# Kernel tuning notes

Measured on AMD Instinct MI355X. Metric: run time of the kernel, lower is better.

The kernel has to match this reference:

```python
import jax, jax.numpy as jnp
import numpy as np

UNITS = 1024
D = 1024

def setup_inputs() -> dict:
    key = jax.random.key(0)
    ks = jax.random.split(key, 8)
    B, T = 32, 2048
    query = jax.random.normal(ks[0], (B, D), dtype=jnp.float32)
    values = jax.random.normal(ks[1], (B, T, D), dtype=jnp.float32)
    s1 = 1.0 / np.sqrt(D)
    s2 = 1.0 / np.sqrt(UNITS)
    W1 = jax.random.normal(ks[2], (D, UNITS), dtype=jnp.float32) * s1
    b1 = jnp.zeros((UNITS,), dtype=jnp.float32)
    W2 = jax.random.normal(ks[3], (D, UNITS), dtype=jnp.float32) * s1
    b2 = jnp.zeros((UNITS,), dtype=jnp.float32)
    Wv = jax.random.normal(ks[4], (UNITS, 1), dtype=jnp.float32) * s2
    bv = jnp.zeros((1,), dtype=jnp.float32)
    return {"query": query, "values": values, "W1": W1, "b1": b1,
            "W2": W2, "b2": b2, "Wv": Wv, "bv": bv}

def reference(query, values, W1, b1, W2, b2, Wv, bv):
    # query: [B, D]; values: [B, T, D]
    q_proj = query @ W1 + b1                     # [B, U]
    v_proj = jnp.einsum('btd,du->btu', values, W2) + b2  # [B, T, U]
    h = jnp.tanh(q_proj[:, None, :] + v_proj)    # [B, T, U]
    score = jnp.einsum('btu,uo->bto', h, Wv) + bv  # [B, T, 1]
    attention_weights = jax.nn.softmax(score, axis=1)  # [B, T, 1]
    context_vector = jnp.sum(attention_weights * values, axis=1)  # [B, D]
    return (context_vector, attention_weights)
```

## Files before the change

### kernel.cpp

```cpp
#include <hip/hip_runtime.h>
#include <hip/hip_bf16.h>
#include <stdint.h>


typedef unsigned short ushort_t;
typedef short bf16x8 __attribute__((ext_vector_type(8)));
typedef float f32x4 __attribute__((ext_vector_type(4)));

#define GLOBAL_AS __attribute__((address_space(1)))
#define LDS_AS    __attribute__((address_space(3)))

__device__ __forceinline__ ushort_t f2bf(float f) {
    union { float f; unsigned int u; } v;
    v.f = f;
    unsigned int u = v.u;
    unsigned int r = u + 0x7FFFu + ((u >> 16) & 1u);
    return (ushort_t)(r >> 16);
}
__device__ __forceinline__ unsigned int pk2(float a, float b) {
    union { __hip_bfloat162 h; unsigned int u; } c;
    c.h = __float22bfloat162_rn(make_float2(a, b));
    return c.u;
}
__device__ __forceinline__ float fast_tanh(float x) {
    float ax = __builtin_fabsf(x);
    float e = __expf(-2.0f * ax);
    float t = (1.0f - e) * __builtin_amdgcn_rcpf(1.0f + e);
    return __builtin_copysignf(t, x);
}

static constexpr int B_ = 32, T_ = 2048, D_ = 1024, U_ = 1024;
static constexpr int M_ = B_ * T_;

__global__ __launch_bounds__(256) void k_convert(const float* __restrict__ v,
                                                 ushort_t* __restrict__ o) {
    size_t i = ((size_t)blockIdx.x * 256 + threadIdx.x) * 8;
    f32x4 a = *(const f32x4*)(v + i);
    f32x4 b = *(const f32x4*)(v + i + 4);
    uint4 p;
    p.x = pk2(a[0], a[1]);
    p.y = pk2(a[2], a[3]);
    p.z = pk2(b[0], b[1]);
    p.w = pk2(b[2], b[3]);
    *(uint4*)(o + i) = p;
}

__global__ __launch_bounds__(256) void k_transpose_w2(const float* __restrict__ W2,
                                                      ushort_t* __restrict__ W2T) {
    __shared__ float tile[32][33];
    int u0 = blockIdx.x * 32, d0 = blockIdx.y * 32;
    int tx = threadIdx.x & 31, ty = threadIdx.x >> 5;
#pragma unroll
    for (int r = 0; r < 4; ++r) {
        int dd = ty + r * 8;
        tile[dd][tx] = W2[(size_t)(d0 + dd) * U_ + (u0 + tx)];
    }
    __syncthreads();
#pragma unroll
    for (int r = 0; r < 4; ++r) {
        int uu = ty + r * 8;
        W2T[(size_t)(u0 + uu) * D_ + (d0 + tx)] = f2bf(tile[tx][uu]);
    }
}

__global__ __launch_bounds__(256) void k_qproj(const float* __restrict__ query,
                                               const float* __restrict__ W1,
                                               const float* __restrict__ b1,
                                               const float* __restrict__ b2,
                                               float* __restrict__ qpb) {
    int b = blockIdx.y;
    int u = blockIdx.x * 256 + threadIdx.x;
    __shared__ float qs[D_];
    for (int i = threadIdx.x; i < D_; i += 256) qs[i] = query[b * D_ + i];
    __syncthreads();
    float acc = 0.f;
#pragma unroll 8
    for (int d = 0; d < D_; ++d) acc += qs[d] * W1[(size_t)d * U_ + u];
    qpb[b * U_ + u] = acc + b1[u] + b2[u];
}

#define BM 128
#define BN 128
#define BK 64

__global__ __launch_bounds__(256) void k_score_gemm(const ushort_t* __restrict__ Vbf,
                                                    const ushort_t* __restrict__ W2T,
                                                    const float* __restrict__ qpb,
                                                    const float* __restrict__ Wv,
                                                    float* __restrict__ scores_partial) {
    __shared__ ushort_t As[BM * BK];
    __shared__ ushort_t Bs[BN * BK];
    __shared__ float sScore[BM];

    const int tid = threadIdx.x;
    const int lane = tid & 63;
    const int w = tid >> 6;
    const int wm = w >> 1;
    const int wn = w & 1;

    const int g = blockIdx.x;
    const int mt = ((g >> 6) << 3) | (g & 7);
    const int nt = (g >> 3) & 7;
    const int m0 = mt * BM;
    const int n0 = nt * BN;

    if (tid < BM) sScore[tid] = 0.f;

    f32x4 acc[4][4];
#pragma unroll
    for (int i = 0; i < 4; ++i)
#pragma unroll
        for (int j = 0; j < 4; ++j) acc[i][j] = (f32x4){0.f, 0.f, 0.f, 0.f};

    const int lr = lane >> 3;
    const int c = (lane & 7) ^ lr;
    const ushort_t* aBase = Vbf + (size_t)(m0 + w * 8 + lr) * D_ + c * 8;
    const ushort_t* bBase = W2T + (size_t)(n0 + w * 8 + lr) * D_ + c * 8;

    const int quad = lane >> 4;
    const int l15 = lane & 15;
    const int l7 = l15 & 7;

    for (int k0 = 0; k0 < D_; k0 += BK) {
#pragma unroll
        for (int i = 0; i < 4; ++i) {
            __builtin_amdgcn_global_load_lds(
                (const GLOBAL_AS void*)(aBase + k0 + (size_t)i * 32 * D_),
                (LDS_AS void*)(As + i * 2048 + w * 512), 16, 0, 0);
        }
#pragma unroll
        for (int i = 0; i < 4; ++i) {
            __builtin_amdgcn_global_load_lds(
                (const GLOBAL_AS void*)(bBase + k0 + (size_t)i * 32 * D_),
                (LDS_AS void*)(Bs + i * 2048 + w * 512), 16, 0, 0);
        }
        __syncthreads();
#pragma unroll
        for (int kk = 0; kk < BK; kk += 32) {
            bf16x8 af[4], bfr[4];
            const int cb = kk >> 3;
#pragma unroll
            for (int i = 0; i < 4; ++i) {
                int r = wm * 64 + i * 16 + l15;
                af[i] = *(const bf16x8*)(As + (r << 6) + ((((quad + cb) ^ l7)) << 3));
            }
#pragma unroll
            for (int j = 0; j < 4; ++j) {
                int r = wn * 64 + j * 16 + l15;
                bfr[j] = *(const bf16x8*)(Bs + (r << 6) + ((((quad + cb) ^ l7)) << 3));
            }
#pragma unroll
            for (int i = 0; i < 4; ++i)
#pragma unroll
                for (int j = 0; j < 4; ++j)
                    acc[i][j] = __builtin_amdgcn_mfma_f32_16x16x32_bf16(
                        af[i], bfr[j], acc[i][j], 0, 0, 0);
        }
        __syncthreads();
    }

    const int b = m0 >> 11;
    const float* qp = qpb + b * U_;
    float qv[4], wv[4];
#pragma unroll
    for (int j = 0; j < 4; ++j) {
        int u = n0 + wn * 64 + j * 16 + l15;
        qv[j] = qp[u];
        wv[j] = Wv[u];
    }
#pragma unroll
    for (int i = 0; i < 4; ++i) {
#pragma unroll
        for (int r = 0; r < 4; ++r) {
            float s = 0.f;
#pragma unroll
            for (int j = 0; j < 4; ++j) s += fast_tanh(acc[i][j][r] + qv[j]) * wv[j];
            s += __shfl_xor(s, 1);
            s += __shfl_xor(s, 2);
            s += __shfl_xor(s, 4);
            s += __shfl_xor(s, 8);
            if (l15 == 0) atomicAdd(&sScore[wm * 64 + i * 16 + quad * 4 + r], s);
        }
    }
    __syncthreads();
    if (tid < BM) scores_partial[(size_t)(m0 + tid) * 8 + nt] = sScore[tid];
}

__global__ __launch_bounds__(256) void k_score_gemm_f32(const float* __restrict__ values,
                                                        const ushort_t* __restrict__ W2T,
                                                        const float* __restrict__ qpb,
                                                        const float* __restrict__ Wv,
                                                        float* __restrict__ scores_partial) {
    __shared__ ushort_t As[BM * BK];
    __shared__ ushort_t Bs[BN * BK];
    __shared__ float sScore[BM];

    const int tid = threadIdx.x;
    const int lane = tid & 63;
    const int w = tid >> 6;
    const int wm = w >> 1;
    const int wn = w & 1;
    const int n0 = blockIdx.x * BN;
    const int m0 = blockIdx.y * BM;

    if (tid < BM) sScore[tid] = 0.f;

    f32x4 acc[4][4];
#pragma unroll
    for (int i = 0; i < 4; ++i)
#pragma unroll
        for (int j = 0; j < 4; ++j) acc[i][j] = (f32x4){0.f, 0.f, 0.f, 0.f};

    const int rr = tid >> 4;
    const int cc = tid & 15;
    const float* aSrc = values + (size_t)(m0 + rr) * D_ + cc * 4;
    ushort_t* aDst = As + rr * BK + cc * 4;

    const int mB = lane >> 3;
    const int kB = (lane & 7) * 8;
    const ushort_t* bBase = W2T + (size_t)(n0 + w * 8 + mB) * D_ + kB;

    const int quad = lane >> 4;
    const int l15 = lane & 15;

    for (int k0 = 0; k0 < D_; k0 += BK) {
#pragma unroll
        for (int i = 0; i < 4; ++i) {
            __builtin_amdgcn_global_load_lds(
                (const GLOBAL_AS void*)(bBase + k0 + (size_t)i * 32 * D_),
                (LDS_AS void*)(Bs + i * 2048 + w * 512), 16, 0, 0);
        }
#pragma unroll
        for (int i = 0; i < 8; ++i) {
            f32x4 v = *(const f32x4*)(aSrc + k0 + (size_t)i * 16 * D_);
            uint2 p;
            p.x = pk2(v[0], v[1]);
            p.y = pk2(v[2], v[3]);
            *(uint2*)(aDst + i * 16 * BK) = p;
        }
        __syncthreads();
#pragma unroll
        for (int kk = 0; kk < BK; kk += 32) {
            bf16x8 af[4], bfr[4];
            const int col = kk + quad * 8;
#pragma unroll
            for (int i = 0; i < 4; ++i)
                af[i] = *(const bf16x8*)(As + (wm * 64 + i * 16 + l15) * BK + col);
#pragma unroll
            for (int j = 0; j < 4; ++j)
                bfr[j] = *(const bf16x8*)(Bs + (wn * 64 + j * 16 + l15) * BK + col);
#pragma unroll
            for (int i = 0; i < 4; ++i)
#pragma unroll
                for (int j = 0; j < 4; ++j)
                    acc[i][j] = __builtin_amdgcn_mfma_f32_16x16x32_bf16(
                        af[i], bfr[j], acc[i][j], 0, 0, 0);
        }
        __syncthreads();
    }

    const int b = m0 >> 11;
    const float* qp = qpb + b * U_;
    float qv[4], wv[4];
#pragma unroll
    for (int j = 0; j < 4; ++j) {
        int u = n0 + wn * 64 + j * 16 + l15;
        qv[j] = qp[u];
        wv[j] = Wv[u];
    }
#pragma unroll
    for (int i = 0; i < 4; ++i) {
#pragma unroll
        for (int r = 0; r < 4; ++r) {
            float s = 0.f;
#pragma unroll
            for (int j = 0; j < 4; ++j) s += fast_tanh(acc[i][j][r] + qv[j]) * wv[j];
            s += __shfl_xor(s, 1);
            s += __shfl_xor(s, 2);
            s += __shfl_xor(s, 4);
            s += __shfl_xor(s, 8);
            if (l15 == 0) atomicAdd(&sScore[wm * 64 + i * 16 + quad * 4 + r], s);
        }
    }
    __syncthreads();
    if (tid < BM) scores_partial[(size_t)(m0 + tid) * 8 + blockIdx.x] = sScore[tid];
}

__global__ __launch_bounds__(256) void k_softmax(const float* __restrict__ scores_partial,
                                                 const float* __restrict__ bv,
                                                 float* __restrict__ w_f,
                                                 float* __restrict__ out_w) {
    const int b = blockIdx.x;
    __shared__ float s[T_];
    __shared__ float red[4];
    const int tid = threadIdx.x;
    const float bvf = bv[0];

    float lmax = -1e30f;
    for (int t = tid; t < T_; t += 256) {
        const float* p = scores_partial + (size_t)(b * T_ + t) * 8;
        float sc = ((p[0] + p[1]) + (p[2] + p[3])) + ((p[4] + p[5]) + (p[6] + p[7])) + bvf;
        s[t] = sc;
        lmax = fmaxf(lmax, sc);
    }
    for (int off = 32; off; off >>= 1) lmax = fmaxf(lmax, __shfl_xor(lmax, off));
    if ((tid & 63) == 0) red[tid >> 6] = lmax;
    __syncthreads();
    const float gmax = fmaxf(fmaxf(red[0], red[1]), fmaxf(red[2], red[3]));

    float lsum = 0.f;
    for (int t = tid; t < T_; t += 256) {
        float e = __expf(s[t] - gmax);
        s[t] = e;
        lsum += e;
    }
    for (int off = 32; off; off >>= 1) lsum += __shfl_xor(lsum, off);
    __syncthreads();
    if ((tid & 63) == 0) red[tid >> 6] = lsum;
    __syncthreads();
    const float ginv = 1.f / ((red[0] + red[1]) + (red[2] + red[3]));

    for (int t = tid; t < T_; t += 256) {
        float wgt = s[t] * ginv;
        w_f[b * T_ + t] = wgt;
        out_w[b * T_ + t] = wgt;
    }
}

__global__ __launch_bounds__(256) void k_ctx_partial(const float* __restrict__ values,
                                                     const float* __restrict__ w_f,
                                                     float* __restrict__ ctx_partial) {
    const int tc = blockIdx.x;
    const int b = blockIdx.y;
    const int tid = threadIdx.x;
    __shared__ float wls[128];
    if (tid < 128) wls[tid] = w_f[b * T_ + tc * 128 + tid];
    __syncthreads();

    f32x4 acc = (f32x4){0.f, 0.f, 0.f, 0.f};
    const float* base = values + (size_t)(b * T_ + tc * 128) * D_ + tid * 4;
#pragma unroll 4
    for (int tt = 0; tt < 128; ++tt) {
        acc += wls[tt] * *(const f32x4*)(base + (size_t)tt * D_);
    }
    *(f32x4*)(ctx_partial + (size_t)(b * 16 + tc) * D_ + tid * 4) = acc;
}

__global__ __launch_bounds__(256) void k_ctx_reduce(const float* __restrict__ ctx_partial,
                                                    float* __restrict__ out_ctx) {
    const int b = blockIdx.x;
    const int d = blockIdx.y * 256 + threadIdx.x;
    float s = 0.f;
#pragma unroll
    for (int p = 0; p < 16; ++p) s += ctx_partial[(size_t)(b * 16 + p) * D_ + d];
    out_ctx[b * D_ + d] = s;
}

extern "C" void kernel_launch(void* const* d_in, const int* in_sizes, int n_in,
                              void* d_out, int out_size, void* d_ws, size_t ws_size,
                              hipStream_t stream) {
    const float* query  = (const float*)d_in[0];
    const float* values = (const float*)d_in[1];
    const float* W1     = (const float*)d_in[2];
    const float* b1     = (const float*)d_in[3];
    const float* W2     = (const float*)d_in[4];
    const float* b2     = (const float*)d_in[5];
    const float* Wv     = (const float*)d_in[6];
    const float* bv     = (const float*)d_in[7];

    float* out_ctx = (float*)d_out;
    float* out_w   = out_ctx + B_ * D_;

    char* ws = (char*)d_ws;
    const size_t OFF_W2T = 0;
    const size_t OFF_QPB = 0x200000;
    const size_t OFF_SP  = 0x220000;
    const size_t OFF_WF  = 0x420000;
    const size_t OFF_CP  = 0x460000;
    const size_t OFF_VBF = 0x660000;
    const size_t NEED    = OFF_VBF + (size_t)M_ * D_ * sizeof(ushort_t);

    ushort_t* W2T            = (ushort_t*)(ws + OFF_W2T);
    float*    qpb            = (float*)(ws + OFF_QPB);
    float*    scores_partial = (float*)(ws + OFF_SP);
    float*    w_f            = (float*)(ws + OFF_WF);
    float*    ctx_partial    = (float*)(ws + OFF_CP);
    ushort_t* Vbf            = (ushort_t*)(ws + OFF_VBF);

    k_transpose_w2<<<dim3(U_ / 32, D_ / 32), 256, 0, stream>>>(W2, W2T);
    k_qproj<<<dim3(U_ / 256, B_), 256, 0, stream>>>(query, W1, b1, b2, qpb);

    if (ws_size >= NEED) {
        k_convert<<<dim3(M_ * D_ / (256 * 8)), 256, 0, stream>>>(values, Vbf);
        k_score_gemm<<<dim3((M_ / BM) * (U_ / BN)), 256, 0, stream>>>(
            Vbf, W2T, qpb, Wv, scores_partial);
    } else {
        k_score_gemm_f32<<<dim3(U_ / BN, M_ / BM), 256, 0, stream>>>(
            values, W2T, qpb, Wv, scores_partial);
    }

    k_softmax<<<dim3(B_), 256, 0, stream>>>(scores_partial, bv, w_f, out_w);
    k_ctx_partial<<<dim3(16, B_), 256, 0, stream>>>(values, w_f, ctx_partial);
    k_ctx_reduce<<<dim3(B_, D_ / 256), 256, 0, stream>>>(ctx_partial, out_ctx);

    (void)in_sizes; (void)n_in; (void)out_size; (void)ws_size;
}
```

Measured before the change: 689.3 us.

## Fuse prep kernels, load GEMM operands directly to registers, read bf16 values for context

Merges the values conversion, W2 transpose and query projection into one k_prep launch, and splits the qproj dot product across four waves to raise parallelism. The bf16 score GEMM drops LDS staging: each wave loads its MFMA fragments straight from global memory into registers with double buffering, with a launch bound of 3 blocks per CU. The context pass now reads the bf16 copy of values instead of fp32, halving its traffic at some precision cost. The register-direct GEMM loads are uncoalesced 16-byte reads with no reuse across waves through LDS, so global and L2 traffic could rise.

```diff
diff --git a/kernel.cpp b/kernel.cpp
--- a/kernel.cpp
+++ b/kernel.cpp
@@ -7,9 +7,11 @@
 typedef short bf16x8 __attribute__((ext_vector_type(8)));
 typedef float f32x4 __attribute__((ext_vector_type(4)));
 
-#define GLOBAL_AS __attribute__((address_space(1)))
-#define LDS_AS    __attribute__((address_space(3)))
-
+__device__ __forceinline__ float bf2f(ushort_t h) {
+    union { unsigned int u; float f; } v;
+    v.u = ((unsigned int)h) << 16;
+    return v.f;
+}
 __device__ __forceinline__ ushort_t f2bf(float f) {
     union { float f; unsigned int u; } v;
     v.f = f;
@@ -31,80 +33,96 @@
 
 static constexpr int B_ = 32, T_ = 2048, D_ = 1024, U_ = 1024;
 static constexpr int M_ = B_ * T_;
-
-__global__ __launch_bounds__(256) void k_convert(const float* __restrict__ v,
-                                                 ushort_t* __restrict__ o) {
-    size_t i = ((size_t)blockIdx.x * 256 + threadIdx.x) * 8;
-    f32x4 a = *(const f32x4*)(v + i);
-    f32x4 b = *(const f32x4*)(v + i + 4);
-    uint4 p;
-    p.x = pk2(a[0], a[1]);
-    p.y = pk2(a[2], a[3]);
-    p.z = pk2(b[0], b[1]);
-    p.w = pk2(b[2], b[3]);
-    *(uint4*)(o + i) = p;
-}
-
-__global__ __launch_bounds__(256) void k_transpose_w2(const float* __restrict__ W2,
-                                                      ushort_t* __restrict__ W2T) {
-    __shared__ float tile[32][33];
-    int u0 = blockIdx.x * 32, d0 = blockIdx.y * 32;
-    int tx = threadIdx.x & 31, ty = threadIdx.x >> 5;
-#pragma unroll
-    for (int r = 0; r < 4; ++r) {
-        int dd = ty + r * 8;
-        tile[dd][tx] = W2[(size_t)(d0 + dd) * U_ + (u0 + tx)];
-    }
-    __syncthreads();
-#pragma unroll
-    for (int r = 0; r < 4; ++r) {
-        int uu = ty + r * 8;
-        W2T[(size_t)(u0 + uu) * D_ + (d0 + tx)] = f2bf(tile[tx][uu]);
-    }
-}
-
-__global__ __launch_bounds__(256) void k_qproj(const float* __restrict__ query,
-                                               const float* __restrict__ W1,
-                                               const float* __restrict__ b1,
-                                               const float* __restrict__ b2,
-                                               float* __restrict__ qpb) {
-    int b = blockIdx.y;
-    int u = blockIdx.x * 256 + threadIdx.x;
-    __shared__ float qs[D_];
-    for (int i = threadIdx.x; i < D_; i += 256) qs[i] = query[b * D_ + i];
-    __syncthreads();
+static constexpr int CONV_B = M_ * D_ / (256 * 8);
+static constexpr int TRANS_B = 1024;
+static constexpr int QPROJ_B = 512;
+
+__global__ __launch_bounds__(256) void k_prep(const float* __restrict__ values,
+                                              const float* __restrict__ W2,
+                                              const float* __restrict__ query,
+                                              const float* __restrict__ W1,
+                                              const float* __restrict__ b1,
+                                              const float* __restrict__ b2,
+                                              ushort_t* __restrict__ Vbf,
+                                              ushort_t* __restrict__ W2T,
+                                              float* __restrict__ qpb,
+                                              int conv_blocks) {
+    __shared__ float smem[1280];
+    int bid = blockIdx.x;
+    const int tid = threadIdx.x;
+
+    if (bid < conv_blocks) {
+        size_t i = ((size_t)bid * 256 + tid) * 8;
+        f32x4 a = *(const f32x4*)(values + i);
+        f32x4 b = *(const f32x4*)(values + i + 4);
+        uint4 p;
+        p.x = pk2(a[0], a[1]);
+        p.y = pk2(a[2], a[3]);
+        p.z = pk2(b[0], b[1]);
+        p.w = pk2(b[2], b[3]);
+        *(uint4*)(Vbf + i) = p;
+        return;
+    }
+    bid -= conv_blocks;
+
+    if (bid < TRANS_B) {
+        float(*tile)[33] = (float(*)[33])smem;
+        int u0 = (bid & 31) * 32, d0 = (bid >> 5) * 32;
+        int tx = tid & 31, ty = tid >> 5;
+#pragma unroll
+        for (int r = 0; r < 4; ++r)
+            tile[ty + r * 8][tx] = W2[(size_t)(d0 + ty + r * 8) * U_ + (u0 + tx)];
+        __syncthreads();
+#pragma unroll
+        for (int r = 0; r < 4; ++r)
+            W2T[(size_t)(u0 + ty + r * 8) * D_ + (d0 + tx)] = f2bf(tile[tx][ty + r * 8]);
+        return;
+    }
+    bid -= TRANS_B;
+
+    const int b = bid >> 4, uc = bid & 15;
+    float* qs = smem;
+    float* red = smem + 1024;
+    for (int i = tid; i < D_; i += 256) qs[i] = query[b * D_ + i];
+    __syncthreads();
+    const int ul = tid & 63, ds = tid >> 6;
+    const int u = uc * 64 + ul;
     float acc = 0.f;
 #pragma unroll 8
-    for (int d = 0; d < D_; ++d) acc += qs[d] * W1[(size_t)d * U_ + u];
-    qpb[b * U_ + u] = acc + b1[u] + b2[u];
+    for (int d = ds * 256; d < ds * 256 + 256; ++d)
+        acc += qs[d] * W1[(size_t)d * U_ + u];
+    red[tid] = acc;
+    __syncthreads();
+    if (tid < 64) {
+        int uu = uc * 64 + tid;
+        qpb[b * U_ + uu] = red[tid] + red[tid + 64] + red[tid + 128] + red[tid + 192] +
+                           b1[uu] + b2[uu];
+    }
 }
 
 #define BM 128
 #define BN 128
-#define BK 64
-
-__global__ __launch_bounds__(256) void k_score_gemm(const ushort_t* __restrict__ Vbf,
-                                                    const ushort_t* __restrict__ W2T,
-                                                    const float* __restrict__ qpb,
-                                                    const float* __restrict__ Wv,
-                                                    float* __restrict__ scores_partial) {
-    __shared__ ushort_t As[BM * BK];
-    __shared__ ushort_t Bs[BN * BK];
+
+__global__ __launch_bounds__(256, 3) void k_score_gemm(const ushort_t* __restrict__ Vbf,
+                                                       const ushort_t* __restrict__ W2T,
+                                                       const float* __restrict__ qpb,
+                                                       const float* __restrict__ Wv,
+                                                       float* __restrict__ scores_partial) {
     __shared__ float sScore[BM];
 
     const int tid = threadIdx.x;
     const int lane = tid & 63;
     const int w = tid >> 6;
-    const int wm = w >> 1;
-    const int wn = w & 1;
+    const int wm = w >> 1, wn = w & 1;
+    const int quad = lane >> 4, l15 = lane & 15;
 
     const int g = blockIdx.x;
     const int mt = ((g >> 6) << 3) | (g & 7);
     const int nt = (g >> 3) & 7;
-    const int m0 = mt * BM;
-    const int n0 = nt * BN;
+    const int m0 = mt * BM, n0 = nt * BN;
 
     if (tid < BM) sScore[tid] = 0.f;
+    __syncthreads();
 
     f32x4 acc[4][4];
 #pragma unroll
@@ -112,51 +130,38 @@
 #pragma unroll
         for (int j = 0; j < 4; ++j) acc[i][j] = (f32x4){0.f, 0.f, 0.f, 0.f};
 
-    const int lr = lane >> 3;
-    const int c = (lane & 7) ^ lr;
-    const ushort_t* aBase = Vbf + (size_t)(m0 + w * 8 + lr) * D_ + c * 8;
-    const ushort_t* bBase = W2T + (size_t)(n0 + w * 8 + lr) * D_ + c * 8;
-
-    const int quad = lane >> 4;
-    const int l15 = lane & 15;
-    const int l7 = l15 & 7;
-
-    for (int k0 = 0; k0 < D_; k0 += BK) {
-#pragma unroll
-        for (int i = 0; i < 4; ++i) {
-            __builtin_amdgcn_global_load_lds(
-                (const GLOBAL_AS void*)(aBase + k0 + (size_t)i * 32 * D_),
-                (LDS_AS void*)(As + i * 2048 + w * 512), 16, 0, 0);
-        }
-#pragma unroll
-        for (int i = 0; i < 4; ++i) {
-            __builtin_amdgcn_global_load_lds(
-                (const GLOBAL_AS void*)(bBase + k0 + (size_t)i * 32 * D_),
-                (LDS_AS void*)(Bs + i * 2048 + w * 512), 16, 0, 0);
-        }
-        __syncthreads();
-#pragma unroll
-        for (int kk = 0; kk < BK; kk += 32) {
-            bf16x8 af[4], bfr[4];
-            const int cb = kk >> 3;
-#pragma unroll
-            for (int i = 0; i < 4; ++i) {
-                int r = wm * 64 + i * 16 + l15;
-                af[i] = *(const bf16x8*)(As + (r << 6) + ((((quad + cb) ^ l7)) << 3));
-            }
-#pragma unroll
-            for (int j = 0; j < 4; ++j) {
-                int r = wn * 64 + j * 16 + l15;
-                bfr[j] = *(const bf16x8*)(Bs + (r << 6) + ((((quad + cb) ^ l7)) << 3));
-            }
-#pragma unroll
-            for (int i = 0; i < 4; ++i)
-#pragma unroll
-                for (int j = 0; j < 4; ++j)
-                    acc[i][j] = __builtin_amdgcn_mfma_f32_16x16x32_bf16(
-                        af[i], bfr[j], acc[i][j], 0, 0, 0);
-        }
-        __syncthreads();
+    const ushort_t* aBase = Vbf + (size_t)(m0 + wm * 64 + l15) * D_ + quad * 8;
+    const ushort_t* bBase = W2T + (size_t)(n0 + wn * 64 + l15) * D_ + quad * 8;
+
+    bf16x8 a0[4], b0[4], a1[4], b1[4];
+#pragma unroll
+    for (int i = 0; i < 4; ++i) a0[i] = *(const bf16x8*)(aBase + i * 16 * D_);
+#pragma unroll
+    for (int j = 0; j < 4; ++j) b0[j] = *(const bf16x8*)(bBase + j * 16 * D_);
+
+    for (int k0 = 0; k0 < D_; k0 += 64) {
+        const int k1 = k0 + 32;
+#pragma unroll
+        for (int i = 0; i < 4; ++i) a1[i] = *(const bf16x8*)(aBase + k1 + i * 16 * D_);
+#pragma unroll
+        for (int j = 0; j < 4; ++j) b1[j] = *(const bf16x8*)(bBase + k1 + j * 16 * D_);
+#pragma unroll
+        for (int i = 0; i < 4; ++i)
+#pragma unroll
+            for (int j = 0; j < 4; ++j)
+                acc[i][j] = __builtin_amdgcn_mfma_f32_16x16x32_bf16(a0[i], b0[j],
+                                                                    acc[i][j], 0, 0, 0);
+        const int k2 = (k0 + 64) & (D_ - 1);
+#pragma unroll
+        for (int i = 0; i < 4; ++i) a0[i] = *(const bf16x8*)(aBase + k2 + i * 16 * D_);
+#pragma unroll
+        for (int j = 0; j < 4; ++j) b0[j] = *(const bf16x8*)(bBase + k2 + j * 16 * D_);
+#pragma unroll
+        for (int i = 0; i < 4; ++i)
+#pragma unroll
+            for (int j = 0; j < 4; ++j)
+                acc[i][j] = __builtin_amdgcn_mfma_f32_16x16x32_bf16(a1[i], b1[j],
+                                                                    acc[i][j], 0, 0, 0);
     }
 
     const int b = m0 >> 11;
@@ -185,6 +190,10 @@
     __syncthreads();
     if (tid < BM) scores_partial[(size_t)(m0 + tid) * 8 + nt] = sScore[tid];
 }
+
+#define BK 64
+#define GLOBAL_AS __attribute__((address_space(1)))
+#define LDS_AS    __attribute__((address_space(3)))
 
 __global__ __launch_bounds__(256) void k_score_gemm_f32(const float* __restrict__ values,
                                                         const ushort_t* __restrict__ W2T,
@@ -198,8 +207,7 @@
     const int tid = threadIdx.x;
     const int lane = tid & 63;
     const int w = tid >> 6;
-    const int wm = w >> 1;
-    const int wn = w & 1;
+    const int wm = w >> 1, wn = w & 1;
     const int n0 = blockIdx.x * BN;
     const int m0 = blockIdx.y * BM;
 
@@ -327,9 +335,44 @@
     }
 }
 
-__global__ __launch_bounds__(256) void k_ctx_partial(const float* __restrict__ values,
-                                                     const float* __restrict__ w_f,
-                                                     float* __restrict__ ctx_partial) {
+__global__ __launch_bounds__(256) void k_ctx_partial_bf(const ushort_t* __restrict__ Vbf,
+                                                        const float* __restrict__ w_f,
+                                                        float* __restrict__ ctx_partial) {
+    const int tc = blockIdx.x;
+    const int b = blockIdx.y;
+    const int tid = threadIdx.x;
+    __shared__ float wls[128];
+    __shared__ float racc[128 * 8];
+    if (tid < 128) wls[tid] = w_f[b * T_ + tc * 128 + tid];
+    __syncthreads();
+
+    const int dg = tid & 127, th = tid >> 7;
+    const int d0 = dg * 8;
+    float acc[8] = {0.f, 0.f, 0.f, 0.f, 0.f, 0.f, 0.f, 0.f};
+    const ushort_t* base = Vbf + (size_t)(b * T_ + tc * 128) * D_ + d0;
+    for (int tt = th; tt < 128; tt += 2) {
+        const float wgt = wls[tt];
+        bf16x8 v = *(const bf16x8*)(base + (size_t)tt * D_);
+#pragma unroll
+        for (int i = 0; i < 8; ++i) acc[i] += wgt * bf2f((ushort_t)v[i]);
+    }
+    if (th == 1) {
+#pragma unroll
+        for (int i = 0; i < 8; ++i) racc[dg * 8 + i] = acc[i];
+    }
+    __syncthreads();
+    if (th == 0) {
+#pragma unroll
+        for (int i = 0; i < 8; ++i) acc[i] += racc[dg * 8 + i];
+        float* out = ctx_partial + (size_t)(b * 16 + tc) * D_ + d0;
+        *(f32x4*)out = (f32x4){acc[0], acc[1], acc[2], acc[3]};
+        *(f32x4*)(out + 4) = (f32x4){acc[4], acc[5], acc[6], acc[7]};
+    }
+}
+
+__global__ __launch_bounds__(256) void k_ctx_partial_f32(const float* __restrict__ values,
+                                                         const float* __restrict__ w_f,
+                                                         float* __restrict__ ctx_partial) {
     const int tc = blockIdx.x;
     const int b = blockIdx.y;
     const int tid = threadIdx.x;
@@ -340,9 +383,8 @@
     f32x4 acc = (f32x4){0.f, 0.f, 0.f, 0.f};
     const float* base = values + (size_t)(b * T_ + tc * 128) * D_ + tid * 4;
 #pragma unroll 4
-    for (int tt = 0; tt < 128; ++tt) {
+    for (int tt = 0; tt < 128; ++tt)
         acc += wls[tt] * *(const f32x4*)(base + (size_t)tt * D_);
-    }
     *(f32x4*)(ctx_partial + (size_t)(b * 16 + tc) * D_ + tid * 4) = acc;
 }
 
@@ -387,20 +429,21 @@
     float*    ctx_partial    = (float*)(ws + OFF_CP);
     ushort_t* Vbf            = (ushort_t*)(ws + OFF_VBF);
 
-    k_transpose_w2<<<dim3(U_ / 32, D_ / 32), 256, 0, stream>>>(W2, W2T);
-    k_qproj<<<dim3(U_ / 256, B_), 256, 0, stream>>>(query, W1, b1, b2, qpb);
-
     if (ws_size >= NEED) {
-        k_convert<<<dim3(M_ * D_ / (256 * 8)), 256, 0, stream>>>(values, Vbf);
+        k_prep<<<dim3(CONV_B + TRANS_B + QPROJ_B), 256, 0, stream>>>(
+            values, W2, query, W1, b1, b2, Vbf, W2T, qpb, CONV_B);
         k_score_gemm<<<dim3((M_ / BM) * (U_ / BN)), 256, 0, stream>>>(
             Vbf, W2T, qpb, Wv, scores_partial);
+        k_softmax<<<dim3(B_), 256, 0, stream>>>(scores_partial, bv, w_f, out_w);
+        k_ctx_partial_bf<<<dim3(16, B_), 256, 0, stream>>>(Vbf, w_f, ctx_partial);
     } else {
+        k_prep<<<dim3(TRANS_B + QPROJ_B), 256, 0, stream>>>(
+            values, W2, query, W1, b1, b2, Vbf, W2T, qpb, 0);
         k_score_gemm_f32<<<dim3(U_ / BN, M_ / BM), 256, 0, stream>>>(
             values, W2T, qpb, Wv, scores_partial);
-    }
-
-    k_softmax<<<dim3(B_), 256, 0, stream>>>(scores_partial, bv, w_f, out_w);
-    k_ctx_partial<<<dim3(16, B_), 256, 0, stream>>>(values, w_f, ctx_partial);
+        k_softmax<<<dim3(B_), 256, 0, stream>>>(scores_partial, bv, w_f, out_w);
+        k_ctx_partial_f32<<<dim3(16, B_), 256, 0, stream>>>(values, w_f, ctx_partial);
+    }
     k_ctx_reduce<<<dim3(B_, D_ / 256), 256, 0, stream>>>(ctx_partial, out_ctx);
 
     (void)in_sizes; (void)n_in; (void)out_size; (void)ws_size;
```

Result: slower. 895.8 us (+30.0%).
